# Optimization experiments

Hardware: AMD Instinct MI355X
Metric: run time of the kernel (lower is better)

Reference implementation:

```python
import jax, jax.numpy as jnp
import numpy as np

N = 100_000      # nodes
E = 3_200_000    # edges (avg degree 32)
F_IN = 128       # num_features
DIM = 10         # hidden dim (module default)
B = 1000         # graphs in the batch


def setup_inputs() -> dict:
    key = jax.random.key(0)
    k1, k2, k3, k4, k5, k6 = jax.random.split(key, 6)
    x = jax.random.normal(k1, (N, F_IN), dtype=jnp.float32)
    edge_index = jax.random.randint(k2, (2, E), 0, N)
    batch = jnp.sort(jax.random.randint(k3, (N,), 0, B))
    # SAGEConv with concat=True has weight shape [2*in, out], no bias
    W1 = jax.random.normal(k4, (2 * F_IN, DIM), dtype=jnp.float32) * 0.05
    W2 = jax.random.normal(k5, (2 * DIM, DIM), dtype=jnp.float32) * 0.1
    Wfc = jax.random.normal(k6, (DIM, 1), dtype=jnp.float32) * 0.1
    return {"x": x, "edge_index": edge_index, "batch": batch,
            "W1": W1, "W2": W2, "Wfc": Wfc}


def _segment_mean(vals, idx, num_segments):
    s = jax.ops.segment_sum(vals, idx, num_segments=num_segments)
    c = jax.ops.segment_sum(jnp.ones((vals.shape[0],), vals.dtype), idx,
                            num_segments=num_segments)
    return s / jnp.maximum(c, 1.0)[:, None]


def _sage_conv(x, src, dst, W):
    # message = x[src]; mean-aggregate into dst; cat([x, aggr]) @ W
    aggr = _segment_mean(x[src], dst, N)          # [N, F]
    return jnp.concatenate([x, aggr], axis=-1) @ W  # [N, out]


def reference(x, edge_index, batch, W1, W2, Wfc):
    src, dst = edge_index[0], edge_index[1]
    h = jax.nn.relu(_sage_conv(x, src, dst, W1))   # [N, DIM]
    h = _sage_conv(h, src, dst, W2)                # [N, DIM]
    g = _segment_mean(h, batch, B)                 # [B, DIM] global_mean_pool
    return jax.nn.sigmoid(g @ Wfc)                 # [B, 1]
```

## Files before the change

kernel.cpp:

```cpp
#include <hip/hip_runtime.h>
#include <cstdint>

typedef unsigned int u32;
typedef unsigned short u16;

#define N_NODES 100000
#define N_EDGES 3200000
#define F_IN 128
#define DIM 10
#define QB 16
#define HPAD 12
#define B_GRAPHS 1000
#define NBLK_N 391

#define SHIFTC 7
#define NBINS 128
#define NCB 782
#define CAPC 4608
#define CHUNK_C 8192
#define NBLK_C 391
#define GSTRIDE 16
#define SEGW 129

__device__ __forceinline__ u16 f2b(float f) {
  union { float f; u32 i; } c; c.f = f;
  u32 r = c.i + 0x7FFFu + ((c.i >> 16) & 1u);
  return (u16)(r >> 16);
}
__device__ __forceinline__ float bl(u32 u) {
  union { u32 i; float f; } c; c.i = u << 16; return c.f;
}
__device__ __forceinline__ float bh(u32 u) {
  union { u32 i; float f; } c; c.i = u & 0xFFFF0000u; return c.f;
}

__device__ __forceinline__ void gemm_body(
    int bid, int tid,
    const float* __restrict__ x, const float* __restrict__ W,
    float* __restrict__ p1, u16* __restrict__ q1b)
{
  int i = bid * 256 + tid;
  if (i >= N_NODES) return;
  const float4* __restrict__ xr = (const float4*)(x + (size_t)i * F_IN);
  float ap[DIM], aq[DIM];
  #pragma unroll
  for (int j = 0; j < DIM; ++j) { ap[j] = 0.f; aq[j] = 0.f; }
  #pragma unroll 4
  for (int k4 = 0; k4 < F_IN / 4; ++k4) {
    float4 v = xr[k4];
    const float* __restrict__ w0 = W + (k4 * 4) * DIM;
    const float* __restrict__ w1 = W + (F_IN + k4 * 4) * DIM;
    #pragma unroll
    for (int j = 0; j < DIM; ++j) {
      ap[j] += v.x * w0[j] + v.y * w0[DIM + j] + v.z * w0[2 * DIM + j] + v.w * w0[3 * DIM + j];
      aq[j] += v.x * w1[j] + v.y * w1[DIM + j] + v.z * w1[2 * DIM + j] + v.w * w1[3 * DIM + j];
    }
  }
  float* pr = p1 + (size_t)i * DIM;
  #pragma unroll
  for (int j = 0; j < DIM; ++j) pr[j] = ap[j];
  u32* qr = (u32*)(q1b + (size_t)i * QB);
  uint4 v0; u32 v1;
  v0.x = (u32)f2b(aq[0]) | ((u32)f2b(aq[1]) << 16);
  v0.y = (u32)f2b(aq[2]) | ((u32)f2b(aq[3]) << 16);
  v0.z = (u32)f2b(aq[4]) | ((u32)f2b(aq[5]) << 16);
  v0.w = (u32)f2b(aq[6]) | ((u32)f2b(aq[7]) << 16);
  v1   = (u32)f2b(aq[8]) | ((u32)f2b(aq[9]) << 16);
  *(uint4*)qr = v0;
  qr[4] = v1;
}

__device__ __forceinline__ void coarse_body(
    int bid, int tid,
    const int* __restrict__ src, const int* __restrict__ dst,
    u32* __restrict__ gcurc, u32* __restrict__ coarse)
{
  __shared__ u32 srt[CHUNK_C];
  __shared__ u32 segst[NCB + 1];
  __shared__ u32 rank[NCB];
  __shared__ u32 gbase[NCB];
  __shared__ u32 wtot[4];

  for (int t = tid; t < NCB; t += 256) rank[t] = 0u;
  __syncthreads();

  int base = bid * CHUNK_C;
  const int4* __restrict__ dst4 = (const int4*)dst;
  const int4* __restrict__ src4 = (const int4*)src;
  #pragma unroll
  for (int it = 0; it < CHUNK_C / 1024; ++it) {
    int e = base + it * 1024 + tid * 4;
    if (e < N_EDGES) {
      int4 d = dst4[(base >> 2) + it * 256 + tid];
      atomicAdd(&rank[(u32)d.x >> SHIFTC], 1u);
      atomicAdd(&rank[(u32)d.y >> SHIFTC], 1u);
      atomicAdd(&rank[(u32)d.z >> SHIFTC], 1u);
      atomicAdd(&rank[(u32)d.w >> SHIFTC], 1u);
    }
  }
  __syncthreads();

  u32 lh[4] = {0u, 0u, 0u, 0u};
  u32 lsum = 0u;
  if (tid < 196) {
    #pragma unroll
    for (int k = 0; k < 4; ++k) {
      int b4 = tid * 4 + k;
      lh[k] = (b4 < NCB) ? rank[b4] : 0u;
      lsum += lh[k];
    }
  }
  u32 v = lsum;
  #pragma unroll
  for (int off = 1; off < 64; off <<= 1) {
    u32 t = __shfl_up(v, off, 64);
    if ((tid & 63) >= off) v += t;
  }
  if ((tid & 63) == 63) wtot[tid >> 6] = v;
  __syncthreads();
  u32 wofs = 0u;
  #pragma unroll
  for (int w = 0; w < 3; ++w) if ((tid >> 6) > w) wofs += wtot[w];
  if (tid < 196) {
    u32 excl = wofs + v - lsum;
    #pragma unroll
    for (int k = 0; k < 4; ++k) {
      int b4 = tid * 4 + k;
      if (b4 < NCB) segst[b4] = excl;
      excl += lh[k];
    }
    if (tid == 195) segst[NCB] = excl;
  }
  __syncthreads();

  for (int t = tid; t < NCB; t += 256) {
    u32 c = segst[t + 1] - segst[t];
    gbase[t] = c ? atomicAdd(&gcurc[t * GSTRIDE], c) : 0u;
    rank[t] = 0u;
  }
  __syncthreads();

  #pragma unroll
  for (int it = 0; it < CHUNK_C / 1024; ++it) {
    int e = base + it * 1024 + tid * 4;
    if (e < N_EDGES) {
      int4 d = dst4[(base >> 2) + it * 256 + tid];
      int4 s = src4[(base >> 2) + it * 256 + tid];
      #pragma unroll
      for (int q = 0; q < 4; ++q) {
        u32 dd = (u32)((q == 0) ? d.x : (q == 1) ? d.y : (q == 2) ? d.z : d.w);
        u32 ss = (u32)((q == 0) ? s.x : (q == 1) ? s.y : (q == 2) ? s.z : s.w);
        u32 cb = dd >> SHIFTC;
        u32 pos = segst[cb] + atomicAdd(&rank[cb], 1u);
        srt[pos] = ((dd & (NBINS - 1u)) << 17) | ss;
      }
    }
  }
  __syncthreads();

  int grp = tid >> 4, lane = tid & 15;
  for (int cb = grp; cb < NCB; cb += 16) {
    u32 st = segst[cb];
    u32 cnt = segst[cb + 1] - st;
    u32 gb = gbase[cb];
    for (u32 r = lane; r < cnt; r += 16u) {
      u32 p = gb + r;
      if (p < CAPC)
        coarse[(size_t)cb * CAPC + p] = srt[st + r];
    }
  }
}

__global__ __launch_bounds__(256) void k_front(
    const int* __restrict__ src, const int* __restrict__ dst,
    u32* __restrict__ gcurc, u32* __restrict__ coarse,
    const float* __restrict__ x, const float* __restrict__ W,
    float* __restrict__ p1, u16* __restrict__ q1b)
{
  if (blockIdx.x < NBLK_C)
    coarse_body(blockIdx.x, threadIdx.x, src, dst, gcurc, coarse);
  else
    gemm_body(blockIdx.x - NBLK_C, threadIdx.x, x, W, p1, q1b);
}

#define SEG_GATHER(QSRC)                                                      \
  float s[DIM];                                                               \
  _Pragma("unroll")                                                           \
  for (int j = 0; j < DIM; ++j) s[j] = 0.f;                                   \
  {                                                                           \
    int k = st + l;                                                           \
    for (; k + 8 < en; k += 16) {                                             \
      int s0 = (int)srt[k], s1 = (int)srt[k + 8];                             \
      const u32* __restrict__ q0 = (const u32*)(QSRC + (size_t)s0 * QB);      \
      const u32* __restrict__ q1 = (const u32*)(QSRC + (size_t)s1 * QB);      \
      uint4 A0 = *(const uint4*)q0; u32 B0 = q0[4];                           \
      uint4 A1 = *(const uint4*)q1; u32 B1 = q1[4];                           \
      s[0] += bl(A0.x) + bl(A1.x); s[1] += bh(A0.x) + bh(A1.x);               \
      s[2] += bl(A0.y) + bl(A1.y); s[3] += bh(A0.y) + bh(A1.y);               \
      s[4] += bl(A0.z) + bl(A1.z); s[5] += bh(A0.z) + bh(A1.z);               \
      s[6] += bl(A0.w) + bl(A1.w); s[7] += bh(A0.w) + bh(A1.w);               \
      s[8] += bl(B0) + bl(B1);     s[9] += bh(B0) + bh(B1);                   \
    }                                                                         \
    if (k < en) {                                                             \
      int s0 = (int)srt[k];                                                   \
      const u32* __restrict__ q0 = (const u32*)(QSRC + (size_t)s0 * QB);      \
      uint4 A0 = *(const uint4*)q0; u32 B0 = q0[4];                           \
      s[0] += bl(A0.x); s[1] += bh(A0.x);                                     \
      s[2] += bl(A0.y); s[3] += bh(A0.y);                                     \
      s[4] += bl(A0.z); s[5] += bh(A0.z);                                     \
      s[6] += bl(A0.w); s[7] += bh(A0.w);                                     \
      s[8] += bl(B0);   s[9] += bh(B0);                                       \
    }                                                                         \
  }                                                                           \
  _Pragma("unroll")                                                           \
  for (int m = 1; m < 8; m <<= 1) {                                           \
    _Pragma("unroll")                                                         \
    for (int j = 0; j < DIM; ++j) s[j] += __shfl_xor(s[j], m, 8);             \
  }

__global__ __launch_bounds__(512) void k_lay1(
    const u32* __restrict__ gcurc, u32* __restrict__ coarse,
    const float* __restrict__ p1, const u16* __restrict__ q1b,
    const float* __restrict__ W2,
    float* __restrict__ p2, u16* __restrict__ q2b,
    u32* __restrict__ segg)
{
  __shared__ u32 lrec[CAPC];
  __shared__ u32 srt[CAPC];
  __shared__ u32 hist[NBINS];
  __shared__ u32 segst[NBINS + 1];
  __shared__ u32 rank[NBINS];
  __shared__ u32 wtot[2];
  __shared__ float w[2 * DIM * DIM];
  int tid = threadIdx.x;
  int c = blockIdx.x;
  for (int t = tid; t < 2 * DIM * DIM; t += 512) w[t] = W2[t];
  if (tid < NBINS) { hist[tid] = 0u; rank[tid] = 0u; }
  __syncthreads();
  int n = min((int)gcurc[c * GSTRIDE], CAPC);
  const u32* __restrict__ rc = coarse + (size_t)c * CAPC;
  for (int r = tid; r < n; r += 512) {
    u32 v = rc[r];
    lrec[r] = v;
    atomicAdd(&hist[(v >> 17) & (NBINS - 1u)], 1u);
  }
  __syncthreads();
  if (tid < NBINS) {
    u32 h = hist[tid];
    u32 v = h;
    #pragma unroll
    for (int off = 1; off < 64; off <<= 1) {
      u32 t = __shfl_up(v, off, 64);
      if ((tid & 63) >= off) v += t;
    }
    if ((tid & 63) == 63) wtot[tid >> 6] = v;
    segst[tid] = v - h;
  }
  __syncthreads();
  if (tid >= 64 && tid < NBINS) segst[tid] += wtot[0];
  if (tid == 0) segst[NBINS] = wtot[0] + wtot[1];
  __syncthreads();
  for (int r = tid; r < n; r += 512) {
    u32 v = lrec[r];
    u32 dl = (v >> 17) & (NBINS - 1u);
    u32 pos = segst[dl] + atomicAdd(&rank[dl], 1u);
    srt[pos] = v & 0x1FFFFu;
  }
  __syncthreads();
  for (int r = tid; r < n; r += 512) coarse[(size_t)c * CAPC + r] = srt[r];
  if (tid <= NBINS) segg[(size_t)c * SEGW + tid] = segst[tid];
  int g0 = tid >> 3, l = tid & 7;
  #pragma unroll
  for (int rd = 0; rd < 2; ++rd) {
    int g2 = rd * 64 + g0;
    int st = (int)segst[g2], en = (int)segst[g2 + 1];
    SEG_GATHER(q1b)
    if (l == 0) {
      int i = c * NBINS + g2;
      if (i < N_NODES) {
        float inv = 1.0f / fmaxf((float)(en - st), 1.0f);
        const float* __restrict__ pr = p1 + (size_t)i * DIM;
        float h[DIM];
        #pragma unroll
        for (int j = 0; j < DIM; ++j) h[j] = fmaxf(pr[j] + s[j] * inv, 0.0f);
        float aa[DIM], bb[DIM];
        #pragma unroll
        for (int j = 0; j < DIM; ++j) {
          float t0 = 0.f, t1 = 0.f;
          #pragma unroll
          for (int kk = 0; kk < DIM; ++kk) {
            t0 += h[kk] * w[kk * DIM + j];
            t1 += h[kk] * w[(DIM + kk) * DIM + j];
          }
          aa[j] = t0; bb[j] = t1;
        }
        float* po = p2 + (size_t)i * DIM;
        #pragma unroll
        for (int j = 0; j < DIM; ++j) po[j] = aa[j];
        u32* qo = (u32*)(q2b + (size_t)i * QB);
        uint4 v0; u32 v1;
        v0.x = (u32)f2b(bb[0]) | ((u32)f2b(bb[1]) << 16);
        v0.y = (u32)f2b(bb[2]) | ((u32)f2b(bb[3]) << 16);
        v0.z = (u32)f2b(bb[4]) | ((u32)f2b(bb[5]) << 16);
        v0.w = (u32)f2b(bb[6]) | ((u32)f2b(bb[7]) << 16);
        v1   = (u32)f2b(bb[8]) | ((u32)f2b(bb[9]) << 16);
        *(uint4*)qo = v0;
        qo[4] = v1;
      }
    }
  }
}

__global__ __launch_bounds__(512) void k_lay2(
    const u32* __restrict__ gcurc, const u32* __restrict__ coarse,
    const u32* __restrict__ segg,
    const float* __restrict__ p2, const u16* __restrict__ q2b,
    float* __restrict__ h2)
{
  __shared__ u32 srt[CAPC];
  __shared__ u32 segst[NBINS + 1];
  int tid = threadIdx.x;
  int c = blockIdx.x;
  if (tid <= NBINS) segst[tid] = segg[(size_t)c * SEGW + tid];
  int n = min((int)gcurc[c * GSTRIDE], CAPC);
  const u32* __restrict__ rc = coarse + (size_t)c * CAPC;
  for (int r = tid; r < n; r += 512) srt[r] = rc[r];
  __syncthreads();
  int g0 = tid >> 3, l = tid & 7;
  #pragma unroll
  for (int rd = 0; rd < 2; ++rd) {
    int g2 = rd * 64 + g0;
    int st = (int)segst[g2], en = (int)segst[g2 + 1];
    SEG_GATHER(q2b)
    if (l == 0) {
      int i = c * NBINS + g2;
      if (i < N_NODES) {
        float inv = 1.0f / fmaxf((float)(en - st), 1.0f);
        const float* __restrict__ pr = p2 + (size_t)i * DIM;
        float* ho = h2 + (size_t)i * HPAD;
        #pragma unroll
        for (int j = 0; j < DIM; ++j) ho[j] = pr[j] + s[j] * inv;
      }
    }
  }
}

__global__ __launch_bounds__(64) void k_pool(
    const float* __restrict__ h2, const int* __restrict__ batch,
    const float* __restrict__ Wfc, float* __restrict__ out)
{
  int b = blockIdx.x;
  int lo = 0, hi = N_NODES;
  while (lo < hi) { int m = (lo + hi) >> 1; if (batch[m] < b) lo = m + 1; else hi = m; }
  int start = lo;
  hi = N_NODES;
  while (lo < hi) { int m = (lo + hi) >> 1; if (batch[m] < b + 1) lo = m + 1; else hi = m; }
  int end = lo;
  float sum[DIM];
  #pragma unroll
  for (int j = 0; j < DIM; ++j) sum[j] = 0.f;
  for (int r = start + (int)threadIdx.x; r < end; r += 64) {
    const float4* __restrict__ p = (const float4*)(h2 + (size_t)r * HPAD);
    float4 r0 = p[0], r1 = p[1];
    float2 r2 = *(const float2*)(h2 + (size_t)r * HPAD + 8);
    sum[0] += r0.x; sum[1] += r0.y; sum[2] += r0.z; sum[3] += r0.w;
    sum[4] += r1.x; sum[5] += r1.y; sum[6] += r1.z; sum[7] += r1.w;
    sum[8] += r2.x; sum[9] += r2.y;
  }
  #pragma unroll
  for (int m = 1; m < 64; m <<= 1) {
    #pragma unroll
    for (int j = 0; j < DIM; ++j) sum[j] += __shfl_xor(sum[j], m, 64);
  }
  if (threadIdx.x == 0) {
    float inv = 1.0f / fmaxf((float)(end - start), 1.0f);
    float acc = 0.f;
    #pragma unroll
    for (int j = 0; j < DIM; ++j) acc += sum[j] * inv * Wfc[j];
    out[b] = 1.0f / (1.0f + expf(-acc));
  }
}

extern "C" void kernel_launch(void* const* d_in, const int* in_sizes, int n_in,
                              void* d_out, int out_size, void* d_ws, size_t ws_size,
                              hipStream_t stream)
{
  const float* x     = (const float*)d_in[0];
  const int*   ei    = (const int*)d_in[1];
  const int*   batch = (const int*)d_in[2];
  const float* W1    = (const float*)d_in[3];
  const float* W2    = (const float*)d_in[4];
  const float* Wfc   = (const float*)d_in[5];
  float* out = (float*)d_out;

  const int* src = ei;
  const int* dst = ei + N_EDGES;

  u32* wsp = (u32*)d_ws;
  u32* gcurc  = wsp;
  u32* coarse = wsp + 12544;
  u32* segg   = coarse + (size_t)NCB * CAPC;
  u32* after  = segg + 100928;
  u16*   q1b = (u16*)after;
  float* p1  = (float*)(after + 800000);
  u16*   q2b = (u16*)(after + 1800000);
  float* p2  = (float*)(after + 2600000);
  float* h2  = (float*)(after + 3600000);

  hipMemsetAsync(gcurc, 0, (size_t)NCB * GSTRIDE * sizeof(u32), stream);

  k_front<<<NBLK_C + NBLK_N, 256, 0, stream>>>(src, dst, gcurc, coarse,
                                               x, W1, p1, q1b);
  k_lay1<<<NCB, 512, 0, stream>>>(gcurc, coarse, p1, q1b, W2, p2, q2b, segg);
  k_lay2<<<NCB, 512, 0, stream>>>(gcurc, coarse, segg, p2, q2b, h2);
  k_pool<<<B_GRAPHS, 64, 0, stream>>>(h2, batch, Wfc, out);
}
```

Before: 227.5 us.

## Fuse layer-1 and layer-2 gathers into one persistent kernel with grid barrier

Coarse buckets are doubled to 256 nodes each (391 buckets), and the two middle kernels are merged into one. Each block sorts its bucket once, keeps the sorted edges in shared memory across a software grid-wide barrier, and then runs the layer-2 gather. This drops the write-back and re-read of sorted edges and segment offsets and removes one launch. It relies on all 391 blocks being co-resident, which is checked through the occupancy API, with the old two-kernel path as fallback. The larger buckets use more shared memory per block and can idle CUs while blocks spin at the barrier.

```diff
diff --git a/kernel.cpp b/kernel.cpp
--- a/kernel.cpp
+++ b/kernel.cpp
@@ -13,14 +13,14 @@
 #define B_GRAPHS 1000
 #define NBLK_N 391
 
-#define SHIFTC 7
-#define NBINS 128
-#define NCB 782
-#define CAPC 4608
+#define SHIFTC 8
+#define NBINS 256
+#define NCB 391
+#define CAPC 8960
 #define CHUNK_C 8192
 #define NBLK_C 391
 #define GSTRIDE 16
-#define SEGW 129
+#define SEGW 257
 
 __device__ __forceinline__ u16 f2b(float f) {
   union { float f; u32 i; } c; c.f = f;
@@ -102,7 +102,7 @@
 
   u32 lh[4] = {0u, 0u, 0u, 0u};
   u32 lsum = 0u;
-  if (tid < 196) {
+  if (tid < 98) {
     #pragma unroll
     for (int k = 0; k < 4; ++k) {
       int b4 = tid * 4 + k;
@@ -121,7 +121,7 @@
   u32 wofs = 0u;
   #pragma unroll
   for (int w = 0; w < 3; ++w) if ((tid >> 6) > w) wofs += wtot[w];
-  if (tid < 196) {
+  if (tid < 98) {
     u32 excl = wofs + v - lsum;
     #pragma unroll
     for (int k = 0; k < 4; ++k) {
@@ -129,7 +129,7 @@
       if (b4 < NCB) segst[b4] = excl;
       excl += lh[k];
     }
-    if (tid == 195) segst[NCB] = excl;
+    if (tid == 97) segst[NCB] = excl;
   }
   __syncthreads();
 
@@ -181,6 +181,46 @@
     coarse_body(blockIdx.x, threadIdx.x, src, dst, gcurc, coarse);
   else
     gemm_body(blockIdx.x - NBLK_C, threadIdx.x, x, W, p1, q1b);
+}
+
+__device__ __forceinline__ void sort_bucket(
+    int tid, int n, const u32* __restrict__ rc,
+    u32* lrec, u32* srt, u32* hist, u32* segst, u32* rank, u32* wtot)
+{
+  if (tid < NBINS) { hist[tid] = 0u; rank[tid] = 0u; }
+  __syncthreads();
+  for (int r = tid; r < n; r += 512) {
+    u32 v = rc[r];
+    lrec[r] = v;
+    atomicAdd(&hist[(v >> 17) & (NBINS - 1u)], 1u);
+  }
+  __syncthreads();
+  u32 h = 0u, v = 0u;
+  if (tid < NBINS) {
+    h = hist[tid]; v = h;
+    #pragma unroll
+    for (int off = 1; off < 64; off <<= 1) {
+      u32 t = __shfl_up(v, off, 64);
+      if ((tid & 63) >= off) v += t;
+    }
+    if ((tid & 63) == 63) wtot[tid >> 6] = v;
+  }
+  __syncthreads();
+  if (tid < NBINS) {
+    u32 wofs = 0u;
+    #pragma unroll
+    for (int w2 = 0; w2 < 3; ++w2) if ((tid >> 6) > w2) wofs += wtot[w2];
+    segst[tid] = wofs + v - h;
+  }
+  if (tid == 0) segst[NBINS] = wtot[0] + wtot[1] + wtot[2] + wtot[3];
+  __syncthreads();
+  for (int r = tid; r < n; r += 512) {
+    u32 vv = lrec[r];
+    u32 dl = (vv >> 17) & (NBINS - 1u);
+    u32 pos = segst[dl] + atomicAdd(&rank[dl], 1u);
+    srt[pos] = vv & 0x1FFFFu;
+  }
+  __syncthreads();
 }
 
 #define SEG_GATHER(QSRC)                                                      \
@@ -218,60 +258,13 @@
     for (int j = 0; j < DIM; ++j) s[j] += __shfl_xor(s[j], m, 8);             \
   }
 
-__global__ __launch_bounds__(512) void k_lay1(
-    const u32* __restrict__ gcurc, u32* __restrict__ coarse,
+__device__ __forceinline__ void lay1_gather(
+    int c, int tid, const u32* srt, const u32* segst, const float* w,
     const float* __restrict__ p1, const u16* __restrict__ q1b,
-    const float* __restrict__ W2,
-    float* __restrict__ p2, u16* __restrict__ q2b,
-    u32* __restrict__ segg)
-{
-  __shared__ u32 lrec[CAPC];
-  __shared__ u32 srt[CAPC];
-  __shared__ u32 hist[NBINS];
-  __shared__ u32 segst[NBINS + 1];
-  __shared__ u32 rank[NBINS];
-  __shared__ u32 wtot[2];
-  __shared__ float w[2 * DIM * DIM];
-  int tid = threadIdx.x;
-  int c = blockIdx.x;
-  for (int t = tid; t < 2 * DIM * DIM; t += 512) w[t] = W2[t];
-  if (tid < NBINS) { hist[tid] = 0u; rank[tid] = 0u; }
-  __syncthreads();
-  int n = min((int)gcurc[c * GSTRIDE], CAPC);
-  const u32* __restrict__ rc = coarse + (size_t)c * CAPC;
-  for (int r = tid; r < n; r += 512) {
-    u32 v = rc[r];
-    lrec[r] = v;
-    atomicAdd(&hist[(v >> 17) & (NBINS - 1u)], 1u);
-  }
-  __syncthreads();
-  if (tid < NBINS) {
-    u32 h = hist[tid];
-    u32 v = h;
-    #pragma unroll
-    for (int off = 1; off < 64; off <<= 1) {
-      u32 t = __shfl_up(v, off, 64);
-      if ((tid & 63) >= off) v += t;
-    }
-    if ((tid & 63) == 63) wtot[tid >> 6] = v;
-    segst[tid] = v - h;
-  }
-  __syncthreads();
-  if (tid >= 64 && tid < NBINS) segst[tid] += wtot[0];
-  if (tid == 0) segst[NBINS] = wtot[0] + wtot[1];
-  __syncthreads();
-  for (int r = tid; r < n; r += 512) {
-    u32 v = lrec[r];
-    u32 dl = (v >> 17) & (NBINS - 1u);
-    u32 pos = segst[dl] + atomicAdd(&rank[dl], 1u);
-    srt[pos] = v & 0x1FFFFu;
-  }
-  __syncthreads();
-  for (int r = tid; r < n; r += 512) coarse[(size_t)c * CAPC + r] = srt[r];
-  if (tid <= NBINS) segg[(size_t)c * SEGW + tid] = segst[tid];
+    float* __restrict__ p2, u16* __restrict__ q2b)
+{
   int g0 = tid >> 3, l = tid & 7;
-  #pragma unroll
-  for (int rd = 0; rd < 2; ++rd) {
+  for (int rd = 0; rd < NBINS / 64; ++rd) {
     int g2 = rd * 64 + g0;
     int st = (int)segst[g2], en = (int)segst[g2 + 1];
     SEG_GATHER(q1b)
@@ -311,24 +304,13 @@
   }
 }
 
-__global__ __launch_bounds__(512) void k_lay2(
-    const u32* __restrict__ gcurc, const u32* __restrict__ coarse,
-    const u32* __restrict__ segg,
+__device__ __forceinline__ void lay2_gather(
+    int c, int tid, const u32* srt, const u32* segst,
     const float* __restrict__ p2, const u16* __restrict__ q2b,
     float* __restrict__ h2)
 {
-  __shared__ u32 srt[CAPC];
-  __shared__ u32 segst[NBINS + 1];
-  int tid = threadIdx.x;
-  int c = blockIdx.x;
-  if (tid <= NBINS) segst[tid] = segg[(size_t)c * SEGW + tid];
-  int n = min((int)gcurc[c * GSTRIDE], CAPC);
-  const u32* __restrict__ rc = coarse + (size_t)c * CAPC;
-  for (int r = tid; r < n; r += 512) srt[r] = rc[r];
-  __syncthreads();
   int g0 = tid >> 3, l = tid & 7;
-  #pragma unroll
-  for (int rd = 0; rd < 2; ++rd) {
+  for (int rd = 0; rd < NBINS / 64; ++rd) {
     int g2 = rd * 64 + g0;
     int st = (int)segst[g2], en = (int)segst[g2 + 1];
     SEG_GATHER(q2b)
@@ -345,6 +327,76 @@
   }
 }
 
+__global__ __launch_bounds__(512, 4) void k_mid(
+    const u32* __restrict__ gcurc, const u32* __restrict__ coarse,
+    const float* __restrict__ p1, const u16* __restrict__ q1b,
+    const float* __restrict__ W2, float* __restrict__ p2,
+    u16* __restrict__ q2b, float* __restrict__ h2, u32* bar)
+{
+  __shared__ u32 lrec[CAPC];
+  __shared__ u32 srt[CAPC];
+  __shared__ u32 hist[NBINS];
+  __shared__ u32 segst[NBINS + 1];
+  __shared__ u32 rank[NBINS];
+  __shared__ u32 wtot[4];
+  __shared__ float w[2 * DIM * DIM];
+  int tid = threadIdx.x, c = blockIdx.x;
+  for (int t = tid; t < 2 * DIM * DIM; t += 512) w[t] = W2[t];
+  int n = min((int)gcurc[c * GSTRIDE], CAPC);
+  sort_bucket(tid, n, coarse + (size_t)c * CAPC, lrec, srt, hist, segst, rank, wtot);
+  lay1_gather(c, tid, srt, segst, w, p1, q1b, p2, q2b);
+  __syncthreads();
+  __threadfence();
+  if (tid == 0) {
+    atomicAdd(bar, 1u);
+    while (__hip_atomic_load(bar, __ATOMIC_RELAXED, __HIP_MEMORY_SCOPE_AGENT)
+           < (u32)NCB)
+      __builtin_amdgcn_s_sleep(32);
+  }
+  __syncthreads();
+  __threadfence();
+  lay2_gather(c, tid, srt, segst, p2, q2b, h2);
+}
+
+__global__ __launch_bounds__(512, 4) void k_lay1f(
+    const u32* __restrict__ gcurc, u32* __restrict__ coarse,
+    const float* __restrict__ p1, const u16* __restrict__ q1b,
+    const float* __restrict__ W2, float* __restrict__ p2,
+    u16* __restrict__ q2b, u32* __restrict__ segg)
+{
+  __shared__ u32 lrec[CAPC];
+  __shared__ u32 srt[CAPC];
+  __shared__ u32 hist[NBINS];
+  __shared__ u32 segst[NBINS + 1];
+  __shared__ u32 rank[NBINS];
+  __shared__ u32 wtot[4];
+  __shared__ float w[2 * DIM * DIM];
+  int tid = threadIdx.x, c = blockIdx.x;
+  for (int t = tid; t < 2 * DIM * DIM; t += 512) w[t] = W2[t];
+  int n = min((int)gcurc[c * GSTRIDE], CAPC);
+  sort_bucket(tid, n, coarse + (size_t)c * CAPC, lrec, srt, hist, segst, rank, wtot);
+  for (int r = tid; r < n; r += 512) coarse[(size_t)c * CAPC + r] = srt[r];
+  if (tid <= NBINS) segg[(size_t)c * SEGW + tid] = segst[tid];
+  lay1_gather(c, tid, srt, segst, w, p1, q1b, p2, q2b);
+}
+
+__global__ __launch_bounds__(512, 4) void k_lay2f(
+    const u32* __restrict__ gcurc, const u32* __restrict__ coarse,
+    const u32* __restrict__ segg,
+    const float* __restrict__ p2, const u16* __restrict__ q2b,
+    float* __restrict__ h2)
+{
+  __shared__ u32 srt[CAPC];
+  __shared__ u32 segst[NBINS + 1];
+  int tid = threadIdx.x, c = blockIdx.x;
+  if (tid <= NBINS) segst[tid] = segg[(size_t)c * SEGW + tid];
+  int n = min((int)gcurc[c * GSTRIDE], CAPC);
+  const u32* __restrict__ rc = coarse + (size_t)c * CAPC;
+  for (int r = tid; r < n; r += 512) srt[r] = rc[r];
+  __syncthreads();
+  lay2_gather(c, tid, srt, segst, p2, q2b, h2);
+}
+
 __global__ __launch_bounds__(64) void k_pool(
     const float* __restrict__ h2, const int* __restrict__ batch,
     const float* __restrict__ Wfc, float* __restrict__ out)
@@ -398,20 +450,33 @@
 
   u32* wsp = (u32*)d_ws;
   u32* gcurc  = wsp;
-  u32* coarse = wsp + 12544;
+  u32* bar    = wsp + 6272;
+  u32* coarse = wsp + 6400;
   u32* segg   = coarse + (size_t)NCB * CAPC;
-  u32* after  = segg + 100928;
+  u32* after  = segg + 100608;
   u16*   q1b = (u16*)after;
   float* p1  = (float*)(after + 800000);
   u16*   q2b = (u16*)(after + 1800000);
   float* p2  = (float*)(after + 2600000);
   float* h2  = (float*)(after + 3600000);
 
-  hipMemsetAsync(gcurc, 0, (size_t)NCB * GSTRIDE * sizeof(u32), stream);
+  hipMemsetAsync(wsp, 0, 6400 * sizeof(u32), stream);
 
   k_front<<<NBLK_C + NBLK_N, 256, 0, stream>>>(src, dst, gcurc, coarse,
                                                x, W1, p1, q1b);
-  k_lay1<<<NCB, 512, 0, stream>>>(gcurc, coarse, p1, q1b, W2, p2, q2b, segg);
-  k_lay2<<<NCB, 512, 0, stream>>>(gcurc, coarse, segg, p2, q2b, h2);
+
+  int dev = 0; hipGetDevice(&dev);
+  int nCU = 0;
+  hipDeviceGetAttribute(&nCU, hipDeviceAttributeMultiprocessorCount, dev);
+  int nb = 0;
+  hipOccupancyMaxActiveBlocksPerMultiprocessor(&nb, k_mid, 512, 0);
+  bool fuse = (nb > 0) && ((long)nb * (long)nCU >= (long)NCB);
+
+  if (fuse) {
+    k_mid<<<NCB, 512, 0, stream>>>(gcurc, coarse, p1, q1b, W2, p2, q2b, h2, bar);
+  } else {
+    k_lay1f<<<NCB, 512, 0, stream>>>(gcurc, coarse, p1, q1b, W2, p2, q2b, segg);
+    k_lay2f<<<NCB, 512, 0, stream>>>(gcurc, coarse, segg, p2, q2b, h2);
+  }
   k_pool<<<B_GRAPHS, 64, 0, stream>>>(h2, batch, Wfc, out);
 }
```

After: 325.7 us. +43.1%, slower.

## Fold Wfc into W2 so layer two aggregates scalars and pools atomically

Applied to the files above, without the earlier changes.

Because layer two, mean pooling and the final linear layer are all linear, W2 is pre-multiplied by Wfc to give two 10-vectors. Layer one then writes one scalar for the self term and one for the neighbor term per node, instead of a 10-wide fp32 row and a bf16 row. Layer two gathers a single float per edge rather than 10 bf16 values, and it atomically accumulates per-graph sums, so the padded h2 buffer and the row-wise pool pass go away. The changes are float summation order from atomics, and the neighbor term is now read in fp32 where it used to be rounded to bf16.

```diff
diff --git a/kernel.cpp b/kernel.cpp
--- a/kernel.cpp
+++ b/kernel.cpp
@@ -9,7 +9,6 @@
 #define F_IN 128
 #define DIM 10
 #define QB 16
-#define HPAD 12
 #define B_GRAPHS 1000
 #define NBLK_N 391
 
@@ -221,8 +220,8 @@
 __global__ __launch_bounds__(512) void k_lay1(
     const u32* __restrict__ gcurc, u32* __restrict__ coarse,
     const float* __restrict__ p1, const u16* __restrict__ q1b,
-    const float* __restrict__ W2,
-    float* __restrict__ p2, u16* __restrict__ q2b,
+    const float* __restrict__ W2, const float* __restrict__ Wfc,
+    float* __restrict__ y, float* __restrict__ z,
     u32* __restrict__ segg)
 {
   __shared__ u32 lrec[CAPC];
@@ -231,10 +230,15 @@
   __shared__ u32 segst[NBINS + 1];
   __shared__ u32 rank[NBINS];
   __shared__ u32 wtot[2];
-  __shared__ float w[2 * DIM * DIM];
+  __shared__ float wv[2 * DIM];
   int tid = threadIdx.x;
   int c = blockIdx.x;
-  for (int t = tid; t < 2 * DIM * DIM; t += 512) w[t] = W2[t];
+  if (tid < 2 * DIM) {
+    float sacc = 0.f;
+    #pragma unroll
+    for (int j = 0; j < DIM; ++j) sacc += W2[tid * DIM + j] * Wfc[j];
+    wv[tid] = sacc;
+  }
   if (tid < NBINS) { hist[tid] = 0u; rank[tid] = 0u; }
   __syncthreads();
   int n = min((int)gcurc[c * GSTRIDE], CAPC);
@@ -280,105 +284,64 @@
       if (i < N_NODES) {
         float inv = 1.0f / fmaxf((float)(en - st), 1.0f);
         const float* __restrict__ pr = p1 + (size_t)i * DIM;
-        float h[DIM];
-        #pragma unroll
-        for (int j = 0; j < DIM; ++j) h[j] = fmaxf(pr[j] + s[j] * inv, 0.0f);
-        float aa[DIM], bb[DIM];
+        float yv = 0.f, zv = 0.f;
         #pragma unroll
         for (int j = 0; j < DIM; ++j) {
-          float t0 = 0.f, t1 = 0.f;
-          #pragma unroll
-          for (int kk = 0; kk < DIM; ++kk) {
-            t0 += h[kk] * w[kk * DIM + j];
-            t1 += h[kk] * w[(DIM + kk) * DIM + j];
-          }
-          aa[j] = t0; bb[j] = t1;
+          float h = fmaxf(pr[j] + s[j] * inv, 0.0f);
+          yv += h * wv[j];
+          zv += h * wv[DIM + j];
         }
-        float* po = p2 + (size_t)i * DIM;
-        #pragma unroll
-        for (int j = 0; j < DIM; ++j) po[j] = aa[j];
-        u32* qo = (u32*)(q2b + (size_t)i * QB);
-        uint4 v0; u32 v1;
-        v0.x = (u32)f2b(bb[0]) | ((u32)f2b(bb[1]) << 16);
-        v0.y = (u32)f2b(bb[2]) | ((u32)f2b(bb[3]) << 16);
-        v0.z = (u32)f2b(bb[4]) | ((u32)f2b(bb[5]) << 16);
-        v0.w = (u32)f2b(bb[6]) | ((u32)f2b(bb[7]) << 16);
-        v1   = (u32)f2b(bb[8]) | ((u32)f2b(bb[9]) << 16);
-        *(uint4*)qo = v0;
-        qo[4] = v1;
+        y[i] = yv;
+        z[i] = zv;
       }
     }
   }
 }
 
-__global__ __launch_bounds__(512) void k_lay2(
+__global__ __launch_bounds__(256) void k_lay2(
     const u32* __restrict__ gcurc, const u32* __restrict__ coarse,
     const u32* __restrict__ segg,
-    const float* __restrict__ p2, const u16* __restrict__ q2b,
-    float* __restrict__ h2)
-{
-  __shared__ u32 srt[CAPC];
+    const float* __restrict__ y, const float* __restrict__ z,
+    const int* __restrict__ batch, float* __restrict__ gacc)
+{
   __shared__ u32 segst[NBINS + 1];
-  int tid = threadIdx.x;
-  int c = blockIdx.x;
+  int tid = threadIdx.x, c = blockIdx.x;
   if (tid <= NBINS) segst[tid] = segg[(size_t)c * SEGW + tid];
-  int n = min((int)gcurc[c * GSTRIDE], CAPC);
+  __syncthreads();
   const u32* __restrict__ rc = coarse + (size_t)c * CAPC;
-  for (int r = tid; r < n; r += 512) srt[r] = rc[r];
-  __syncthreads();
   int g0 = tid >> 3, l = tid & 7;
   #pragma unroll
-  for (int rd = 0; rd < 2; ++rd) {
-    int g2 = rd * 64 + g0;
-    int st = (int)segst[g2], en = (int)segst[g2 + 1];
-    SEG_GATHER(q2b)
+  for (int rd = 0; rd < 4; ++rd) {
+    int loc = rd * 32 + g0;
+    int st = (int)segst[loc], en = (int)segst[loc + 1];
+    float sc = 0.f;
+    for (int k = st + l; k < en; k += 8) sc += z[rc[k]];
+    #pragma unroll
+    for (int m = 1; m < 8; m <<= 1) sc += __shfl_xor(sc, m, 8);
     if (l == 0) {
-      int i = c * NBINS + g2;
+      int i = c * NBINS + loc;
       if (i < N_NODES) {
-        float inv = 1.0f / fmaxf((float)(en - st), 1.0f);
-        const float* __restrict__ pr = p2 + (size_t)i * DIM;
-        float* ho = h2 + (size_t)i * HPAD;
-        #pragma unroll
-        for (int j = 0; j < DIM; ++j) ho[j] = pr[j] + s[j] * inv;
+        float val = y[i] + sc / fmaxf((float)(en - st), 1.0f);
+        atomicAdd(&gacc[batch[i]], val);
       }
     }
   }
 }
 
-__global__ __launch_bounds__(64) void k_pool(
-    const float* __restrict__ h2, const int* __restrict__ batch,
-    const float* __restrict__ Wfc, float* __restrict__ out)
-{
-  int b = blockIdx.x;
+__global__ __launch_bounds__(256) void k_pool(
+    const int* __restrict__ batch, const float* __restrict__ gacc,
+    float* __restrict__ out)
+{
+  int b = blockIdx.x * 256 + (int)threadIdx.x;
+  if (b >= B_GRAPHS) return;
   int lo = 0, hi = N_NODES;
   while (lo < hi) { int m = (lo + hi) >> 1; if (batch[m] < b) lo = m + 1; else hi = m; }
   int start = lo;
   hi = N_NODES;
   while (lo < hi) { int m = (lo + hi) >> 1; if (batch[m] < b + 1) lo = m + 1; else hi = m; }
-  int end = lo;
-  float sum[DIM];
-  #pragma unroll
-  for (int j = 0; j < DIM; ++j) sum[j] = 0.f;
-  for (int r = start + (int)threadIdx.x; r < end; r += 64) {
-    const float4* __restrict__ p = (const float4*)(h2 + (size_t)r * HPAD);
-    float4 r0 = p[0], r1 = p[1];
-    float2 r2 = *(const float2*)(h2 + (size_t)r * HPAD + 8);
-    sum[0] += r0.x; sum[1] += r0.y; sum[2] += r0.z; sum[3] += r0.w;
-    sum[4] += r1.x; sum[5] += r1.y; sum[6] += r1.z; sum[7] += r1.w;
-    sum[8] += r2.x; sum[9] += r2.y;
-  }
-  #pragma unroll
-  for (int m = 1; m < 64; m <<= 1) {
-    #pragma unroll
-    for (int j = 0; j < DIM; ++j) sum[j] += __shfl_xor(sum[j], m, 64);
-  }
-  if (threadIdx.x == 0) {
-    float inv = 1.0f / fmaxf((float)(end - start), 1.0f);
-    float acc = 0.f;
-    #pragma unroll
-    for (int j = 0; j < DIM; ++j) acc += sum[j] * inv * Wfc[j];
-    out[b] = 1.0f / (1.0f + expf(-acc));
-  }
+  int cnt = lo - start;
+  float g = gacc[b] / fmaxf((float)cnt, 1.0f);
+  out[b] = 1.0f / (1.0f + expf(-g));
 }
 
 extern "C" void kernel_launch(void* const* d_in, const int* in_sizes, int n_in,
@@ -398,20 +361,20 @@
 
   u32* wsp = (u32*)d_ws;
   u32* gcurc  = wsp;
-  u32* coarse = wsp + 12544;
+  float* gacc = (float*)(wsp + 12544);
+  u32* coarse = wsp + 13568;
   u32* segg   = coarse + (size_t)NCB * CAPC;
   u32* after  = segg + 100928;
   u16*   q1b = (u16*)after;
   float* p1  = (float*)(after + 800000);
-  u16*   q2b = (u16*)(after + 1800000);
-  float* p2  = (float*)(after + 2600000);
-  float* h2  = (float*)(after + 3600000);
-
-  hipMemsetAsync(gcurc, 0, (size_t)NCB * GSTRIDE * sizeof(u32), stream);
+  float* y   = (float*)(after + 1800000);
+  float* z   = (float*)(after + 1900096);
+
+  hipMemsetAsync(wsp, 0, 13568 * sizeof(u32), stream);
 
   k_front<<<NBLK_C + NBLK_N, 256, 0, stream>>>(src, dst, gcurc, coarse,
                                                x, W1, p1, q1b);
-  k_lay1<<<NCB, 512, 0, stream>>>(gcurc, coarse, p1, q1b, W2, p2, q2b, segg);
-  k_lay2<<<NCB, 512, 0, stream>>>(gcurc, coarse, segg, p2, q2b, h2);
-  k_pool<<<B_GRAPHS, 64, 0, stream>>>(h2, batch, Wfc, out);
-}
+  k_lay1<<<NCB, 512, 0, stream>>>(gcurc, coarse, p1, q1b, W2, Wfc, y, z, segg);
+  k_lay2<<<NCB, 256, 0, stream>>>(gcurc, coarse, segg, y, z, batch, gacc);
+  k_pool<<<4, 256, 0, stream>>>(batch, gacc, out);
+}
```

After: 234.6 us. 1.03x slower.
